# Optimization experiments

Hardware: AMD Instinct MI355X
Metric: run time of the kernel (lower is better)

## Reference

```python
import jax, jax.numpy as jnp
import numpy as np

EPS = 1e-5


def _layer_norm(x, w, b):
    mu = jnp.mean(x, axis=-1, keepdims=True)
    var = jnp.mean(jnp.square(x - mu), axis=-1, keepdims=True)
    return (x - mu) * jax.lax.rsqrt(var + EPS) * w + b


def setup_inputs() -> dict:
    key = jax.random.key(0)
    ks = jax.random.split(key, 8)
    b, n, d, h = 1, 512, 128, 128
    edges = jax.random.normal(ks[0], (b, n, n, d), dtype=jnp.float32)
    mask = jax.random.bernoulli(ks[1], 0.9, (b, n, n))  # True = valid
    s = 0.02
    return {
        "edges": edges,
        "mask": mask,
        "ln1_w": jnp.ones((d,), jnp.float32),
        "ln1_b": jnp.zeros((d,), jnp.float32),
        "W_fg": jax.random.normal(ks[2], (4 * h, d), jnp.float32) * s,
        "b_fg": jnp.zeros((4 * h,), jnp.float32),
        "W_go": jax.random.normal(ks[3], (d, d), jnp.float32) * s,
        "b_go": jnp.zeros((d,), jnp.float32),
        "ln2_w": jnp.ones((h,), jnp.float32),
        "ln2_b": jnp.zeros((h,), jnp.float32),
        "W_out": jax.random.normal(ks[4], (d, h), jnp.float32) * s,
        "b_out": jnp.zeros((d,), jnp.float32),
    }


def reference(edges, mask, ln1_w, ln1_b, W_fg, b_fg, W_go, b_go, ln2_w, ln2_b, W_out, b_out):
    h = W_fg.shape[0] // 4
    x = _layer_norm(edges, ln1_w, ln1_b)                         # [b,n,n,d]
    fg = jnp.einsum('bijd,ed->bije', x, W_fg) + b_fg             # [b,n,n,4h]
    feats, gates = fg[..., :2 * h], fg[..., 2 * h:]
    gated = feats * jax.nn.sigmoid(gates)                        # [b,n,n,2h]
    to_feats, from_feats = gated[..., :h], gated[..., h:]
    out_gate = jax.nn.sigmoid(jnp.einsum('bijd,ed->bije', x, W_go) + b_go)
    m = mask[..., None]                                          # True = keep
    to_feats = jnp.where(m, to_feats, 0.0)
    from_feats = jnp.where(m, from_feats, 0.0)
    out_gate = jnp.where(m, out_gate, 0.0)
    # triangle outgoing: contract over shared k axis per channel d
    tri = jnp.einsum('bikd,bjkd->bijd', to_feats, from_feats)    # [b,n,n,h]
    out = jnp.einsum('bijh,dh->bijd', _layer_norm(tri, ln2_w, ln2_b), W_out) + b_out
    return out_gate * out
```

## Files before the change

kernel.cpp:

```cpp
#include <hip/hip_runtime.h>

#define NSEQ 512
#define DCH 128
#define RTOT (NSEQ * NSEQ)

typedef __attribute__((ext_vector_type(8))) short bf16x8;
typedef __attribute__((ext_vector_type(4))) float f32x4;

__device__ __forceinline__ unsigned short f2bf(float v) {
  union { float f; unsigned int u; } x; x.f = v;
  unsigned int u = x.u;
  return (unsigned short)((u + 0x7fffu + ((u >> 16) & 1u)) >> 16);
}
__device__ __forceinline__ float bf2f(unsigned short s) {
  union { unsigned int u; float f; } x; x.u = ((unsigned int)s) << 16;
  return x.f;
}
__device__ __forceinline__ float sigmoidf(float x) { return 1.f / (1.f + __expf(-x)); }

__device__ __forceinline__ void async16(const unsigned short* g, unsigned short* l) {
  __builtin_amdgcn_global_load_lds(
      (const __attribute__((address_space(1))) unsigned int*)g,
      (__attribute__((address_space(3))) unsigned int*)l, 16, 0, 0);
}

__global__ void prep_kernel(const float* __restrict__ W_fg, const float* __restrict__ b_fg,
                            const float* __restrict__ W_go, const float* __restrict__ b_go,
                            const float* __restrict__ W_out,
                            unsigned short* __restrict__ Wc, float* __restrict__ bc,
                            unsigned short* __restrict__ Woutb) {
  int idx = blockIdx.x * 256 + threadIdx.x;
  if (idx < 640 * 128) {
    int rr = idx >> 7, k = idx & 127;
    float v, bv;
    if (rr < 512) {
      int m = rr >> 7;
      int srow = (m == 1) ? rr + 128 : (m == 2) ? rr - 128 : rr;
      v = W_fg[srow * 128 + k];
      bv = b_fg[srow];
    } else {
      int srow = rr - 512;
      v = W_go[srow * 128 + k];
      bv = b_go[srow];
    }
    Wc[idx] = f2bf(v);
    if (k == 0) bc[rr] = bv;
  } else {
    int i2 = idx - 640 * 128;
    if (i2 < 128 * 128) Woutb[i2] = f2bf(W_out[i2]);
  }
}

__global__ __launch_bounds__(256) void ln1_kernel(const float* __restrict__ edges,
                                                  const float* __restrict__ w,
                                                  const float* __restrict__ b,
                                                  unsigned short* __restrict__ xb) {
  int wv = threadIdx.x >> 6;
  int lane = threadIdx.x & 63;
  size_t row = (size_t)blockIdx.x * 4 + wv;
  const float2* e = (const float2*)(edges + row * 128);
  float2 v = e[lane];
  float s = v.x + v.y, sq = v.x * v.x + v.y * v.y;
#pragma unroll
  for (int off = 32; off; off >>= 1) {
    s += __shfl_xor(s, off);
    sq += __shfl_xor(sq, off);
  }
  float mu = s * (1.f / 128.f);
  float var = sq * (1.f / 128.f) - mu * mu;
  float rs = rsqrtf(var + 1e-5f);
  int c = lane * 2;
  float x0 = (v.x - mu) * rs * w[c] + b[c];
  float x1 = (v.y - mu) * rs * w[c + 1] + b[c + 1];
  unsigned int packed = (unsigned int)f2bf(x0) | ((unsigned int)f2bf(x1) << 16);
  ((unsigned int*)(xb + row * 128))[lane] = packed;
}

__global__ __launch_bounds__(256) void fg_gemm_kernel(
    const unsigned short* __restrict__ xb, const unsigned short* __restrict__ Wc,
    const float* __restrict__ bc, const int* __restrict__ mask,
    unsigned short* __restrict__ toT, unsigned short* __restrict__ fromT) {
  __shared__ unsigned int Cs[128 * 36];
  int nb = blockIdx.y;
  int wv = threadIdx.x >> 6, lane = threadIdx.x & 63;
  int qm = lane & 15, quad = lane >> 4;
  int r0 = blockIdx.x * 64;
  int nbase = nb * 256;

  bf16x8 Bf[2][4], Bg[2][4];
#pragma unroll
  for (int ft = 0; ft < 2; ft++)
#pragma unroll
    for (int kk = 0; kk < 4; kk++) {
      int ko = kk * 32 + quad * 8;
      Bf[ft][kk] = *(const bf16x8*)(Wc + (size_t)(nbase + wv * 32 + ft * 16 + qm) * 128 + ko);
      Bg[ft][kk] = *(const bf16x8*)(Wc + (size_t)(nbase + 128 + wv * 32 + ft * 16 + qm) * 128 + ko);
    }

#pragma unroll
  for (int m = 0; m < 4; m++) {
    int rw = r0 + m * 16;
    f32x4 accf[2], accg[2];
#pragma unroll
    for (int ft = 0; ft < 2; ft++) {
      accf[ft] = (f32x4){0.f, 0.f, 0.f, 0.f};
      accg[ft] = (f32x4){0.f, 0.f, 0.f, 0.f};
    }
#pragma unroll
    for (int kk = 0; kk < 4; kk++) {
      int ko = kk * 32 + quad * 8;
      bf16x8 a = *(const bf16x8*)(xb + (size_t)(rw + qm) * 128 + ko);
#pragma unroll
      for (int ft = 0; ft < 2; ft++) {
        accf[ft] = __builtin_amdgcn_mfma_f32_16x16x32_bf16(a, Bf[ft][kk], accf[ft], 0, 0, 0);
        accg[ft] = __builtin_amdgcn_mfma_f32_16x16x32_bf16(a, Bg[ft][kk], accg[ft], 0, 0, 0);
      }
    }
    int rbase = rw + quad * 4;
    int4 mi = *(const int4*)(mask + rbase);
    float mk[4] = {mi.x ? 1.f : 0.f, mi.y ? 1.f : 0.f, mi.z ? 1.f : 0.f, mi.w ? 1.f : 0.f};
#pragma unroll
    for (int ft = 0; ft < 2; ft++) {
      int c = wv * 32 + ft * 16 + qm;
      float bF = bc[nbase + c];
      float bG = bc[nbase + 128 + c];
      float v0 = (accf[ft][0] + bF) * sigmoidf(accg[ft][0] + bG) * mk[0];
      float v1 = (accf[ft][1] + bF) * sigmoidf(accg[ft][1] + bG) * mk[1];
      float v2 = (accf[ft][2] + bF) * sigmoidf(accg[ft][2] + bG) * mk[2];
      float v3 = (accf[ft][3] + bF) * sigmoidf(accg[ft][3] + bG) * mk[3];
      unsigned int u0 = (unsigned int)f2bf(v0) | ((unsigned int)f2bf(v1) << 16);
      unsigned int u1 = (unsigned int)f2bf(v2) | ((unsigned int)f2bf(v3) << 16);
      *(uint2*)(Cs + c * 36 + m * 8 + quad * 2) = (uint2){u0, u1};
    }
  }
  __syncthreads();
  {
    unsigned short* dst = (nb == 0) ? toT : fromT;
    int pl = lane >> 3, lo = lane & 7;
#pragma unroll
    for (int i = 0; i < 4; i++) {
      int p = wv * 32 + i * 8 + pl;
      uint4 v = *(const uint4*)(Cs + p * 36 + lo * 4);
      *(uint4*)(dst + (size_t)p * RTOT + r0 + lo * 8) = v;
    }
  }
}

__global__ __launch_bounds__(256) void go_gemm_kernel(
    const unsigned short* __restrict__ xb, const unsigned short* __restrict__ Wc,
    const float* __restrict__ bc, const int* __restrict__ mask,
    float* __restrict__ gate_out) {
  int wv = threadIdx.x >> 6, lane = threadIdx.x & 63;
  int qm = lane & 15, quad = lane >> 4;
  int rw = blockIdx.x * 64 + wv * 16;

  f32x4 acc[8];
#pragma unroll
  for (int t = 0; t < 8; t++) acc[t] = (f32x4){0.f, 0.f, 0.f, 0.f};

#pragma unroll
  for (int kk = 0; kk < 4; kk++) {
    int ko = kk * 32 + quad * 8;
    bf16x8 a = *(const bf16x8*)(xb + (size_t)(rw + qm) * 128 + ko);
#pragma unroll
    for (int t = 0; t < 8; t++) {
      bf16x8 bf = *(const bf16x8*)(Wc + (size_t)(512 + t * 16 + qm) * 128 + ko);
      acc[t] = __builtin_amdgcn_mfma_f32_16x16x32_bf16(a, bf, acc[t], 0, 0, 0);
    }
  }

  int rbase = rw + quad * 4;
  int4 mi = *(const int4*)(mask + rbase);
  float mk[4] = {mi.x ? 1.f : 0.f, mi.y ? 1.f : 0.f, mi.z ? 1.f : 0.f, mi.w ? 1.f : 0.f};
#pragma unroll
  for (int t = 0; t < 8; t++) {
    int c = t * 16 + qm;
    float bG = bc[512 + c];
#pragma unroll
    for (int reg = 0; reg < 4; reg++) {
      float g = sigmoidf(acc[t][reg] + bG) * mk[reg];
      gate_out[(size_t)(rbase + reg) * 128 + c] = g;
    }
  }
}

__global__ __launch_bounds__(256) void tri_gemm_kernel(
    const unsigned short* __restrict__ toT, const unsigned short* __restrict__ fromT,
    unsigned short* __restrict__ triT) {
  __shared__ unsigned short smem[128 * 136];
  unsigned short* As = smem;
  unsigned short* Bs = smem + 128 * 64;

  int d = blockIdx.z;
  int i0 = blockIdx.x * 128, j0 = blockIdx.y * 128;
  int tid = threadIdx.x, w = tid >> 6, lane = tid & 63;
  int qm = lane & 15, quad = lane >> 4;
  int wm = w >> 1, wn = w & 1;
  const unsigned short* A = toT + (size_t)d * RTOT;
  const unsigned short* B = fromT + (size_t)d * RTOT;
  int lr = lane >> 3, lk = (lane & 7) * 8;

  f32x4 acc[4][4];
#pragma unroll
  for (int m = 0; m < 4; m++)
#pragma unroll
    for (int n = 0; n < 4; n++) acc[m][n] = (f32x4){0.f, 0.f, 0.f, 0.f};

  for (int kb = 0; kb < 512; kb += 64) {
    __syncthreads();
#pragma unroll
    for (int q = 0; q < 4; q++) {
      int blk = w * 4 + q;
      async16(A + (size_t)(i0 + blk * 8 + lr) * 512 + kb + lk, As + blk * 512);
      async16(B + (size_t)(j0 + blk * 8 + lr) * 512 + kb + lk, Bs + blk * 512);
    }
    __syncthreads();
#pragma unroll
    for (int kk = 0; kk < 2; kk++) {
      bf16x8 af[4], bfr[4];
#pragma unroll
      for (int m = 0; m < 4; m++)
        af[m] = *(const bf16x8*)(As + (wm * 64 + m * 16 + qm) * 64 + kk * 32 + quad * 8);
#pragma unroll
      for (int n = 0; n < 4; n++)
        bfr[n] = *(const bf16x8*)(Bs + (wn * 64 + n * 16 + qm) * 64 + kk * 32 + quad * 8);
#pragma unroll
      for (int m = 0; m < 4; m++)
#pragma unroll
        for (int n = 0; n < 4; n++)
          acc[m][n] = __builtin_amdgcn_mfma_f32_16x16x32_bf16(af[m], bfr[n], acc[m][n], 0, 0, 0);
    }
  }

  __syncthreads();
#pragma unroll
  for (int m = 0; m < 4; m++) {
    int rb = wm * 64 + m * 16 + quad * 4;
#pragma unroll
    for (int n = 0; n < 4; n++) {
      int col = wn * 64 + n * 16 + qm;
#pragma unroll
      for (int reg = 0; reg < 4; reg++)
        smem[(rb + reg) * 136 + col] = f2bf(acc[m][n][reg]);
    }
  }
  __syncthreads();
  {
    int row = tid >> 1, half = tid & 1;
    const uint4* src = (const uint4*)(smem + row * 136 + half * 64);
    uint4 v[8];
#pragma unroll
    for (int u = 0; u < 8; u++) v[u] = src[u];
    uint4* dst = (uint4*)(triT + (size_t)d * RTOT + (size_t)(i0 + row) * 512 + j0 + half * 64);
#pragma unroll
    for (int u = 0; u < 8; u++) dst[u] = v[u];
  }
}

__global__ __launch_bounds__(256) void out_kernel(
    const unsigned short* __restrict__ triT, const unsigned short* __restrict__ Woutb,
    const float* __restrict__ ln2w, const float* __restrict__ ln2b,
    const float* __restrict__ b_out, float* __restrict__ out,
    const unsigned short* __restrict__ xb, const unsigned short* __restrict__ Wc,
    const float* __restrict__ bc, const int* __restrict__ mask, int fuse) {
  __shared__ unsigned short nt[64][136];
  __shared__ float mu_s[64], rs_s[64];
  int r0 = blockIdx.x * 64;
  int tid = threadIdx.x;
  int wv = tid >> 6, lane = tid & 63;
  int qm = lane & 15, quad = lane >> 4;

  int dch = tid >> 1, half = tid & 1;
  const uint4* src = (const uint4*)(triT + (size_t)dch * RTOT + r0 + half * 32);
  uint4 sv0 = src[0], sv1 = src[1], sv2 = src[2], sv3 = src[3];

  bf16x8 Bo[2][4], Bg[2][4];
#pragma unroll
  for (int ft = 0; ft < 2; ft++)
#pragma unroll
    for (int kk = 0; kk < 4; kk++) {
      int c = wv * 32 + ft * 16 + qm;
      int ko = kk * 32 + quad * 8;
      Bo[ft][kk] = *(const bf16x8*)(Woutb + (size_t)c * 128 + ko);
      if (fuse) Bg[ft][kk] = *(const bf16x8*)(Wc + (size_t)(512 + c) * 128 + ko);
    }

  int4 mi4[4];
  float bo_[2], bG_[2];
#pragma unroll
  for (int ft = 0; ft < 2; ft++) {
    int c = wv * 32 + ft * 16 + qm;
    bo_[ft] = b_out[c];
    bG_[ft] = fuse ? bc[512 + c] : 0.f;
  }
  if (fuse) {
#pragma unroll
    for (int m = 0; m < 4; m++) mi4[m] = *(const int4*)(mask + r0 + m * 16 + quad * 4);
  }

  const unsigned short* xA = xb + (size_t)(r0 + qm) * 128 + quad * 8;
  bf16x8 a2cur[4], a2nxt[4];
  if (fuse) {
#pragma unroll
    for (int kk = 0; kk < 4; kk++) a2cur[kk] = *(const bf16x8*)(xA + kk * 32);
  }

  {
    uint4 v[4] = {sv0, sv1, sv2, sv3};
    const unsigned short* pv = (const unsigned short*)v;
#pragma unroll
    for (int u = 0; u < 32; u++) nt[half * 32 + u][dch] = pv[u];
  }
  __syncthreads();

  {
    int p = tid >> 2, part = tid & 3;
    float s = 0.f, sq = 0.f;
#pragma unroll
    for (int u = 0; u < 4; u++) {
      bf16x8 v = *(const bf16x8*)(&nt[p][part * 32 + u * 8]);
#pragma unroll
      for (int e = 0; e < 8; e++) {
        float f = bf2f((unsigned short)v[e]);
        s += f; sq += f * f;
      }
    }
    s += __shfl_xor(s, 1); sq += __shfl_xor(sq, 1);
    s += __shfl_xor(s, 2); sq += __shfl_xor(sq, 2);
    float mu = s * (1.f / 128.f);
    float var = sq * (1.f / 128.f) - mu * mu;
    if (part == 0) { mu_s[p] = mu; rs_s[p] = rsqrtf(var + 1e-5f); }
  }
  __syncthreads();

#pragma unroll
  for (int m = 0; m < 4; m++) {
    if (fuse && m < 3) {
#pragma unroll
      for (int kk = 0; kk < 4; kk++)
        a2nxt[kk] = *(const bf16x8*)(xA + (m + 1) * 2048 + kk * 32);
    }

    int rl = m * 16 + qm;
    float mu = mu_s[rl], rs = rs_s[rl];

    bf16x8 afr[4];
#pragma unroll
    for (int kk = 0; kk < 4; kk++) {
      int ko = kk * 32 + quad * 8;
      bf16x8 raw = *(const bf16x8*)(&nt[rl][ko]);
#pragma unroll
      for (int e = 0; e < 8; e++) {
        float wf = ln2w[ko + e], bv = ln2b[ko + e];
        afr[kk][e] = (short)f2bf((bf2f((unsigned short)raw[e]) - mu) * rs * wf + bv);
      }
    }

    f32x4 accO[2], accG[2];
#pragma unroll
    for (int ft = 0; ft < 2; ft++) {
      accO[ft] = (f32x4){0.f, 0.f, 0.f, 0.f};
      accG[ft] = (f32x4){0.f, 0.f, 0.f, 0.f};
    }
#pragma unroll
    for (int kk = 0; kk < 4; kk++) {
#pragma unroll
      for (int ft = 0; ft < 2; ft++)
        accO[ft] = __builtin_amdgcn_mfma_f32_16x16x32_bf16(afr[kk], Bo[ft][kk], accO[ft], 0, 0, 0);
      if (fuse) {
#pragma unroll
        for (int ft = 0; ft < 2; ft++)
          accG[ft] = __builtin_amdgcn_mfma_f32_16x16x32_bf16(a2cur[kk], Bg[ft][kk], accG[ft], 0, 0, 0);
      }
    }

    int rbase = r0 + m * 16 + quad * 4;
    if (fuse) {
      int4 mi = mi4[m];
      float mk[4] = {mi.x ? 1.f : 0.f, mi.y ? 1.f : 0.f, mi.z ? 1.f : 0.f, mi.w ? 1.f : 0.f};
#pragma unroll
      for (int ft = 0; ft < 2; ft++) {
        int c = wv * 32 + ft * 16 + qm;
#pragma unroll
        for (int reg = 0; reg < 4; reg++) {
          float g = sigmoidf(accG[ft][reg] + bG_[ft]) * mk[reg];
          out[(size_t)(rbase + reg) * 128 + c] = (accO[ft][reg] + bo_[ft]) * g;
        }
      }
#pragma unroll
      for (int kk = 0; kk < 4; kk++) a2cur[kk] = a2nxt[kk];
    } else {
#pragma unroll
      for (int ft = 0; ft < 2; ft++) {
        int c = wv * 32 + ft * 16 + qm;
#pragma unroll
        for (int reg = 0; reg < 4; reg++) {
          size_t off = (size_t)(rbase + reg) * 128 + c;
          out[off] = (accO[ft][reg] + bo_[ft]) * out[off];
        }
      }
    }
  }
}

extern "C" void kernel_launch(void* const* d_in, const int* in_sizes, int n_in,
                              void* d_out, int out_size, void* d_ws, size_t ws_size,
                              hipStream_t stream) {
  const float* edges = (const float*)d_in[0];
  const int* mask = (const int*)d_in[1];
  const float* ln1w = (const float*)d_in[2];
  const float* ln1b = (const float*)d_in[3];
  const float* W_fg = (const float*)d_in[4];
  const float* b_fg = (const float*)d_in[5];
  const float* W_go = (const float*)d_in[6];
  const float* b_go = (const float*)d_in[7];
  const float* ln2w = (const float*)d_in[8];
  const float* ln2b = (const float*)d_in[9];
  const float* W_out = (const float*)d_in[10];
  const float* b_out = (const float*)d_in[11];

  char* ws = (char*)d_ws;
  const size_t SZ = (size_t)RTOT * DCH * 2;
  const size_t WSMALL = 0x40000;
  unsigned short* xb = (unsigned short*)ws;
  unsigned short* toT = (unsigned short*)(ws + SZ);
  unsigned short* fromT = (unsigned short*)(ws + 2 * SZ);
  unsigned short* Wc = (unsigned short*)(ws + 3 * SZ);
  float* bc = (float*)(ws + 3 * SZ + 640 * 128 * 2);
  unsigned short* Woutb = (unsigned short*)(ws + 3 * SZ + 640 * 128 * 2 + 640 * 4);
  float* gate = (float*)d_out;

  bool fits = ws_size >= 4 * SZ + WSMALL;
  unsigned short* triT = fits ? (unsigned short*)(ws + 3 * SZ + WSMALL) : xb;

  prep_kernel<<<384, 256, 0, stream>>>(W_fg, b_fg, W_go, b_go, W_out, Wc, bc, Woutb);
  ln1_kernel<<<RTOT / 4, 256, 0, stream>>>(edges, ln1w, ln1b, xb);
  fg_gemm_kernel<<<dim3(RTOT / 64, 2), 256, 0, stream>>>(xb, Wc, bc, mask, toT, fromT);
  if (!fits) go_gemm_kernel<<<RTOT / 64, 256, 0, stream>>>(xb, Wc, bc, mask, gate);
  tri_gemm_kernel<<<dim3(4, 4, 128), 256, 0, stream>>>(toT, fromT, triT);
  out_kernel<<<RTOT / 64, 256, 0, stream>>>(triT, Woutb, ln2w, ln2b, b_out,
                                            (float*)d_out, xb, Wc, bc, mask, fits ? 1 : 0);
}
```

Before: 595.4 us.

## Remap tri-GEMM blocks per XCD and double out_kernel row tile

```diff
diff --git a/kernel.cpp b/kernel.cpp
--- a/kernel.cpp
+++ b/kernel.cpp
@@ -191,8 +191,12 @@
   unsigned short* As = smem;
   unsigned short* Bs = smem + 128 * 64;
 
-  int d = blockIdx.z;
-  int i0 = blockIdx.x * 128, j0 = blockIdx.y * 128;
+  int n = (int)(blockIdx.x + (blockIdx.y << 2) + (blockIdx.z << 4));
+  int xcd = n & 7, s = n >> 3;
+  int d = xcd * 16 + (s >> 4);
+  int xy = s & 15;
+  int i0 = (xy & 3) * 128, j0 = (xy >> 2) * 128;
+
   int tid = threadIdx.x, w = tid >> 6, lane = tid & 63;
   int qm = lane & 15, quad = lane >> 4;
   int wm = w >> 1, wn = w & 1;
@@ -204,7 +208,7 @@
 #pragma unroll
   for (int m = 0; m < 4; m++)
 #pragma unroll
-    for (int n = 0; n < 4; n++) acc[m][n] = (f32x4){0.f, 0.f, 0.f, 0.f};
+    for (int n2 = 0; n2 < 4; n2++) acc[m][n2] = (f32x4){0.f, 0.f, 0.f, 0.f};
 
   for (int kb = 0; kb < 512; kb += 64) {
     __syncthreads();
@@ -222,13 +226,13 @@
       for (int m = 0; m < 4; m++)
         af[m] = *(const bf16x8*)(As + (wm * 64 + m * 16 + qm) * 64 + kk * 32 + quad * 8);
 #pragma unroll
-      for (int n = 0; n < 4; n++)
-        bfr[n] = *(const bf16x8*)(Bs + (wn * 64 + n * 16 + qm) * 64 + kk * 32 + quad * 8);
+      for (int n2 = 0; n2 < 4; n2++)
+        bfr[n2] = *(const bf16x8*)(Bs + (wn * 64 + n2 * 16 + qm) * 64 + kk * 32 + quad * 8);
 #pragma unroll
       for (int m = 0; m < 4; m++)
 #pragma unroll
-        for (int n = 0; n < 4; n++)
-          acc[m][n] = __builtin_amdgcn_mfma_f32_16x16x32_bf16(af[m], bfr[n], acc[m][n], 0, 0, 0);
+        for (int n2 = 0; n2 < 4; n2++)
+          acc[m][n2] = __builtin_amdgcn_mfma_f32_16x16x32_bf16(af[m], bfr[n2], acc[m][n2], 0, 0, 0);
     }
   }
 
@@ -237,11 +241,11 @@
   for (int m = 0; m < 4; m++) {
     int rb = wm * 64 + m * 16 + quad * 4;
 #pragma unroll
-    for (int n = 0; n < 4; n++) {
-      int col = wn * 64 + n * 16 + qm;
+    for (int n2 = 0; n2 < 4; n2++) {
+      int col = wn * 64 + n2 * 16 + qm;
 #pragma unroll
       for (int reg = 0; reg < 4; reg++)
-        smem[(rb + reg) * 136 + col] = f2bf(acc[m][n][reg]);
+        smem[(rb + reg) * 136 + col] = f2bf(acc[m][n2][reg]);
     }
   }
   __syncthreads();
@@ -263,16 +267,18 @@
     const float* __restrict__ b_out, float* __restrict__ out,
     const unsigned short* __restrict__ xb, const unsigned short* __restrict__ Wc,
     const float* __restrict__ bc, const int* __restrict__ mask, int fuse) {
-  __shared__ unsigned short nt[64][136];
-  __shared__ float mu_s[64], rs_s[64];
-  int r0 = blockIdx.x * 64;
+  __shared__ unsigned short nt[128][136];
+  __shared__ float mu_s[128], rs_s[128];
+  int r0 = blockIdx.x * 128;
   int tid = threadIdx.x;
   int wv = tid >> 6, lane = tid & 63;
   int qm = lane & 15, quad = lane >> 4;
 
   int dch = tid >> 1, half = tid & 1;
-  const uint4* src = (const uint4*)(triT + (size_t)dch * RTOT + r0 + half * 32);
-  uint4 sv0 = src[0], sv1 = src[1], sv2 = src[2], sv3 = src[3];
+  const uint4* src = (const uint4*)(triT + (size_t)dch * RTOT + r0 + half * 64);
+  uint4 sv[8];
+#pragma unroll
+  for (int u = 0; u < 8; u++) sv[u] = src[u];
 
   bf16x8 Bo[2][4], Bg[2][4];
 #pragma unroll
@@ -285,7 +291,7 @@
       if (fuse) Bg[ft][kk] = *(const bf16x8*)(Wc + (size_t)(512 + c) * 128 + ko);
     }
 
-  int4 mi4[4];
+  int4 mi4[8];
   float bo_[2], bG_[2];
 #pragma unroll
   for (int ft = 0; ft < 2; ft++) {
@@ -295,7 +301,7 @@
   }
   if (fuse) {
 #pragma unroll
-    for (int m = 0; m < 4; m++) mi4[m] = *(const int4*)(mask + r0 + m * 16 + quad * 4);
+    for (int m = 0; m < 8; m++) mi4[m] = *(const int4*)(mask + r0 + m * 16 + quad * 4);
   }
 
   const unsigned short* xA = xb + (size_t)(r0 + qm) * 128 + quad * 8;
@@ -306,19 +312,18 @@
   }
 
   {
-    uint4 v[4] = {sv0, sv1, sv2, sv3};
-    const unsigned short* pv = (const unsigned short*)v;
-#pragma unroll
-    for (int u = 0; u < 32; u++) nt[half * 32 + u][dch] = pv[u];
+    const unsigned short* pv = (const unsigned short*)sv;
+#pragma unroll
+    for (int u = 0; u < 64; u++) nt[half * 64 + u][dch] = pv[u];
   }
   __syncthreads();
 
   {
-    int p = tid >> 2, part = tid & 3;
+    int p = tid >> 1, part = tid & 1;
     float s = 0.f, sq = 0.f;
 #pragma unroll
-    for (int u = 0; u < 4; u++) {
-      bf16x8 v = *(const bf16x8*)(&nt[p][part * 32 + u * 8]);
+    for (int u = 0; u < 8; u++) {
+      bf16x8 v = *(const bf16x8*)(&nt[p][part * 64 + u * 8]);
 #pragma unroll
       for (int e = 0; e < 8; e++) {
         float f = bf2f((unsigned short)v[e]);
@@ -326,7 +331,6 @@
       }
     }
     s += __shfl_xor(s, 1); sq += __shfl_xor(sq, 1);
-    s += __shfl_xor(s, 2); sq += __shfl_xor(sq, 2);
     float mu = s * (1.f / 128.f);
     float var = sq * (1.f / 128.f) - mu * mu;
     if (part == 0) { mu_s[p] = mu; rs_s[p] = rsqrtf(var + 1e-5f); }
@@ -334,8 +338,8 @@
   __syncthreads();
 
 #pragma unroll
-  for (int m = 0; m < 4; m++) {
-    if (fuse && m < 3) {
+  for (int m = 0; m < 8; m++) {
+    if (fuse && m < 7) {
 #pragma unroll
       for (int kk = 0; kk < 4; kk++)
         a2nxt[kk] = *(const bf16x8*)(xA + (m + 1) * 2048 + kk * 32);
@@ -438,6 +442,6 @@
   fg_gemm_kernel<<<dim3(RTOT / 64, 2), 256, 0, stream>>>(xb, Wc, bc, mask, toT, fromT);
   if (!fits) go_gemm_kernel<<<RTOT / 64, 256, 0, stream>>>(xb, Wc, bc, mask, gate);
   tri_gemm_kernel<<<dim3(4, 4, 128), 256, 0, stream>>>(toT, fromT, triT);
-  out_kernel<<<RTOT / 64, 256, 0, stream>>>(triT, Woutb, ln2w, ln2b, b_out,
-                                            (float*)d_out, xb, Wc, bc, mask, fits ? 1 : 0);
-}
+  out_kernel<<<RTOT / 128, 256, 0, stream>>>(triT, Woutb, ln2w, ln2b, b_out,
+                                             (float*)d_out, xb, Wc, bc, mask, fits ? 1 : 0);
+}
```

Result: faster. 565.6 us (-5.0%).
